# Kernel tuning notes

Hardware: AMD Instinct MI355X
Metric: run time of the kernel (lower is better)

The kernel has to match this reference:

```python
import jax, jax.numpy as jnp
import numpy as np

N_C, N_F = 25000, 100000   # coarse / fine node counts
E_C, E_F = 100000, 400000  # coarse / fine edge counts
W, F_IN, F_OUT = 128, 128, 4


def _fnn2(x, w1, b1, w2, b2):
    # 2-layer FNN (fnns_depth=2) with SELU, dropout=0 (eval)
    return jax.nn.selu(x @ w1 + b1) @ w2 + b2


def _interaction(v, e, src, dst, n, ew1, eb1, ew2, eb2, nw1, nb1, nw2, nb2):
    # InteractionNetwork: edge update (gather) -> mean scatter -> node update, residuals
    e = _fnn2(jnp.concatenate([e, v[src], v[dst]], axis=-1), ew1, eb1, ew2, eb2) + e
    s = jax.ops.segment_sum(e, dst, num_segments=n)
    cnt = jax.ops.segment_sum(jnp.ones((e.shape[0], 1), e.dtype), dst, num_segments=n)
    agg = s / jnp.maximum(cnt, 1.0)  # 'mean' aggregation
    v = _fnn2(jnp.concatenate([v, agg], axis=-1), nw1, nb1, nw2, nb2) + v
    return v, e


def setup_inputs() -> dict:
    key = jax.random.key(0)
    ks = iter(jax.random.split(key, 64))
    def rn(shape, scale=1.0):
        return jax.random.normal(next(ks), shape, jnp.float32) * scale
    s3, s2, s1 = 1.0 / np.sqrt(3 * W), 1.0 / np.sqrt(2 * W), 1.0 / np.sqrt(W)
    d = {
        'v': rn((N_C, F_IN)),
        'c_coarse': rn((N_C, W)), 'c_fine': rn((N_F, W)),
        'e_coarse': rn((E_C, W)), 'e_fine': rn((E_F, W)),
        'rel_dist': rn((N_F, 1)),
        'ei_coarse': jax.random.randint(next(ks), (2, E_C), 0, N_C),
        'ei_fine': jax.random.randint(next(ks), (2, E_F), 0, N_F),
        'cluster': jax.random.randint(next(ks), (N_F,), 0, N_C),
        'in_node_w': rn((F_IN, W), 1.0 / np.sqrt(F_IN)), 'in_node_b': rn((W,), 0.01),
        'cond_w': rn((2, W, W), s1), 'cond_b': rn((2, W), 0.01),
        'edge_in_w': rn((2, W, W), s1), 'edge_in_b': rn((2, W), 0.01),
        'bn_ew1': rn((2, 3 * W, W), s3), 'bn_eb1': rn((2, W), 0.01),
        'bn_ew2': rn((2, W, W), s1), 'bn_eb2': rn((2, W), 0.01),
        'bn_nw1': rn((2, 2 * W, W), s2), 'bn_nb1': rn((2, W), 0.01),
        'bn_nw2': rn((2, W, W), s1), 'bn_nb2': rn((2, W), 0.01),
        'unp_w1': rn((W + 1, W), 1.0 / np.sqrt(W + 1)), 'unp_b1': rn((W,), 0.01),
        'unp_w2': rn((W, W), s1), 'unp_b2': rn((W,), 0.01),
        'up_ew1': rn((2, 3 * W, W), s3), 'up_eb1': rn((2, W), 0.01),
        'up_ew2': rn((2, W, W), s1), 'up_eb2': rn((2, W), 0.01),
        'up_nw1': rn((2, 2 * W, W), s2), 'up_nb1': rn((2, W), 0.01),
        'up_nw2': rn((2, W, W), s1), 'up_nb2': rn((2, W), 0.01),
        'out_w': rn((W, F_OUT), s1), 'out_b': rn((F_OUT,), 0.01),
    }
    return d


def reference(v, c_coarse, c_fine, e_coarse, e_fine, rel_dist, ei_coarse, ei_fine, cluster,
              in_node_w, in_node_b, cond_w, cond_b, edge_in_w, edge_in_b,
              bn_ew1, bn_eb1, bn_ew2, bn_eb2, bn_nw1, bn_nb1, bn_nw2, bn_nb2,
              unp_w1, unp_b1, unp_w2, unp_b2,
              up_ew1, up_eb1, up_ew2, up_eb2, up_nw1, up_nb1, up_nw2, up_nb2,
              out_w, out_b):
    src_c, dst_c = ei_coarse[0], ei_coarse[1]
    src_f, dst_f = ei_fine[0], ei_fine[1]
    # input projection + coarse-scale conditioning
    v = v @ in_node_w + in_node_b
    v = v + (c_coarse @ cond_w[0] + cond_b[0])
    e = e_coarse @ edge_in_w[0] + edge_in_b[0]
    # bottleneck InteractionNetwork blocks on coarse graph
    for i in range(bn_ew1.shape[0]):
        v, e = _interaction(v, e, src_c, dst_c, N_C,
                            bn_ew1[i], bn_eb1[i], bn_ew2[i], bn_eb2[i],
                            bn_nw1[i], bn_nb1[i], bn_nw2[i], bn_nb2[i])
    # up block: project skip conditioning/edges, unpool coarse->fine via cluster gather + FNN on [v, scalar rel pos]
    c = c_fine @ cond_w[1] + cond_b[1]
    e = e_fine @ edge_in_w[1] + edge_in_b[1]
    v = _fnn2(jnp.concatenate([v[cluster], rel_dist], axis=-1), unp_w1, unp_b1, unp_w2, unp_b2)
    v = v + c
    for i in range(up_ew1.shape[0]):
        v, e = _interaction(v, e, src_f, dst_f, N_F,
                            up_ew1[i], up_eb1[i], up_ew2[i], up_eb2[i],
                            up_nw1[i], up_nb1[i], up_nw2[i], up_nb2[i])
    return v @ out_w + out_b
```

## Files before the change

### kernel.cpp

```cpp
#include <hip/hip_runtime.h>
#include <hip/hip_bf16.h>

typedef __bf16 bf16_t;
typedef __bf16 bf16x8 __attribute__((ext_vector_type(8)));
typedef float f32x4 __attribute__((ext_vector_type(4)));

#define SELU_SCALE 1.0507009873554805f
#define SELU_ALPHA 1.6732632423543772f

__device__ __forceinline__ float selu_f(float x) {
    return x > 0.0f ? SELU_SCALE * x : SELU_SCALE * SELU_ALPHA * (__expf(x) - 1.0f);
}

__device__ __forceinline__ int4 load8(const void* p, size_t elem_off, int isf) {
    if (!isf) return *(const int4*)((const bf16_t*)p + elem_off);
    const float* f = (const float*)p + elem_off;
    float4 a = ((const float4*)f)[0], b = ((const float4*)f)[1];
    union { int4 i; bf16_t h[8]; } u;
    u.h[0] = (bf16_t)a.x; u.h[1] = (bf16_t)a.y; u.h[2] = (bf16_t)a.z; u.h[3] = (bf16_t)a.w;
    u.h[4] = (bf16_t)b.x; u.h[5] = (bf16_t)b.y; u.h[6] = (bf16_t)b.z; u.h[7] = (bf16_t)b.w;
    return u.i;
}

__global__ void detect_dtype(const unsigned short* p, int* flag) {
    if (threadIdx.x == 0) {
        float m = 0.0f;
        for (int i = 0; i < 128; i++) {
            unsigned int u = ((unsigned int)p[i]) << 16;
            float v = __uint_as_float(u);
            v = fabsf(v);
            if (!(v <= 1e3f)) { m = 1e30f; break; }
            m = fmaxf(m, v);
        }
        *flag = (m > 1e3f) ? 1 : 0;
    }
}

struct VDesc { const void* s; bf16_t* d; int eoff; int n; };
struct VArgs { VDesc v[19]; };
__global__ void convert_vecs(VArgs a, const int* __restrict__ flag) {
    int isf = *flag;
    VDesc vd = a.v[blockIdx.y];
    int i = blockIdx.x * 256 + threadIdx.x;
    if (i < vd.n) {
        size_t idx = (size_t)vd.eoff + i;
        vd.d[i] = isf ? (bf16_t)(((const float*)vd.s)[idx]) : ((const bf16_t*)vd.s)[idx];
    }
}

struct TDesc { const void* s; bf16_t* d; int eoff; int Ksrc; int Ktot; int koff; };
struct TArgs { TDesc t[31]; };
__global__ void transpose_all(TArgs a, const int* __restrict__ flag) {
    int isf = *flag;
    TDesc td = a.t[blockIdx.y];
    int i = blockIdx.x * 256 + threadIdx.x;
    if (i < 128 * td.Ksrc) {
        int n = i / td.Ksrc;
        int k = i - n * td.Ksrc;
        size_t si = (size_t)td.eoff + (size_t)k * 128 + n;
        bf16_t v = isf ? (bf16_t)(((const float*)td.s)[si]) : ((const bf16_t*)td.s)[si];
        td.d[(size_t)n * td.Ktot + td.koff + k] = v;
    }
}

__global__ void count_dst2(const int* __restrict__ d0, int* __restrict__ c0, int E0,
                           const int* __restrict__ d1, int* __restrict__ c1, int E1) {
    const int* dst = blockIdx.y ? d1 : d0;
    int* cnt = blockIdx.y ? c1 : c0;
    int E = blockIdx.y ? E1 : E0;
    int e = blockIdx.x * 256 + threadIdx.x;
    if (e < E) atomicAdd(&cnt[dst[e]], 1);
}

__global__ void seg_alloc2(const int* __restrict__ c0, int* __restrict__ rp0, int* __restrict__ cu0, int n0,
                           const int* __restrict__ c1, int* __restrict__ rp1, int* __restrict__ cu1, int n1,
                           int* __restrict__ totals) {
    const int* cnt = blockIdx.y ? c1 : c0;
    int* rp = blockIdx.y ? rp1 : rp0;
    int* cu = blockIdx.y ? cu1 : cu0;
    int n = blockIdx.y ? n1 : n0;
    int* total = totals + blockIdx.y;
    int i = blockIdx.x * 256 + threadIdx.x;
    if (i < n) { int s = atomicAdd(total, cnt[i]); rp[i] = s; cu[i] = s; }
}

__global__ void csr_scatter2(const int* __restrict__ d0, int* __restrict__ cu0, int* __restrict__ e0, int E0,
                             const int* __restrict__ d1, int* __restrict__ cu1, int* __restrict__ e1, int E1) {
    const int* dst = blockIdx.y ? d1 : d0;
    int* cur = blockIdx.y ? cu1 : cu0;
    int* eids = blockIdx.y ? e1 : e0;
    int E = blockIdx.y ? E1 : E0;
    int e = blockIdx.x * 256 + threadIdx.x;
    if (e < E) {
        unsigned s = (unsigned)atomicAdd(&cur[dst[e]], 1);
        if (s < (unsigned)E) eids[s] = e;
    }
}

__global__ void permute_ends2(const int* __restrict__ e0, const int* __restrict__ s0,
                              const int* __restrict__ d0, int* __restrict__ sp0,
                              int* __restrict__ dp0, int E0,
                              const int* __restrict__ e1, const int* __restrict__ s1,
                              const int* __restrict__ d1, int* __restrict__ sp1,
                              int* __restrict__ dp1, int E1) {
    const int* eids = blockIdx.y ? e1 : e0;
    const int* src = blockIdx.y ? s1 : s0;
    const int* dst = blockIdx.y ? d1 : d0;
    int* sp = blockIdx.y ? sp1 : sp0;
    int* dp = blockIdx.y ? dp1 : dp0;
    int E = blockIdx.y ? E1 : E0;
    int s = blockIdx.x * 256 + threadIdx.x;
    if (s < E) { int e = eids[s]; sp[s] = src[e]; dp[s] = dst[e]; }
}

template<int K, int N>
__global__ __launch_bounds__(256) void lin1(
    int M, const void* __restrict__ A0, const void* __restrict__ A1,
    const int* __restrict__ gi,
    const bf16_t* __restrict__ Wt, const bf16_t* __restrict__ b1,
    const bf16_t* __restrict__ b2, const bf16_t* __restrict__ res,
    bf16_t* __restrict__ out, const int* __restrict__ flag)
{
    constexpr int SA = K + 8;
    constexpr int NCT = N / 64;
    __shared__ bf16_t sA[64 * SA];
    const int isf = *flag;
    const int tid = threadIdx.x;
    const int row0 = blockIdx.x * 64;
    const int lane16 = tid & 15;
    const int rgrp = tid >> 4;

    #pragma unroll
    for (int chunk = 0; chunk < K; chunk += 128) {
        const void* sp = chunk ? A1 : A0;
        for (int r = rgrp; r < 64; r += 16) {
            int rr = row0 + r; if (rr >= M) rr = M - 1;
            if (gi) rr = gi[rr];
            int4 u = load8(sp, (size_t)rr * 128 + lane16 * 8, isf);
            *(int4*)&sA[r * SA + chunk + lane16 * 8] = u;
        }
    }
    __syncthreads();

    const int lane = tid & 63, wave = tid >> 6;
    const int l15 = lane & 15, lk = lane >> 4;
    const int colbase = wave * (N / 4);
    f32x4 acc[4][NCT];
    const f32x4 zero = {0.f, 0.f, 0.f, 0.f};
    for (int rt = 0; rt < 4; rt++)
        for (int ct = 0; ct < NCT; ct++) acc[rt][ct] = zero;

    #pragma unroll
    for (int k0 = 0; k0 < K; k0 += 32) {
        bf16x8 wv[NCT];
        #pragma unroll
        for (int ct = 0; ct < NCT; ct++)
            wv[ct] = *(const bf16x8*)(Wt + (size_t)(colbase + ct * 16 + l15) * K + k0 + lk * 8);
        #pragma unroll
        for (int rt = 0; rt < 4; rt++) {
            bf16x8 av = *(const bf16x8*)(&sA[(rt * 16 + l15) * SA + k0 + lk * 8]);
            #pragma unroll
            for (int ct = 0; ct < NCT; ct++)
                acc[rt][ct] = __builtin_amdgcn_mfma_f32_16x16x32_bf16(av, wv[ct], acc[rt][ct], 0, 0, 0);
        }
    }

    #pragma unroll
    for (int rt = 0; rt < 4; rt++)
        #pragma unroll
        for (int ct = 0; ct < NCT; ct++) {
            int col = colbase + ct * 16 + l15;
            float bc = (float)b1[col] + (b2 ? (float)b2[col] : 0.0f);
            #pragma unroll
            for (int r = 0; r < 4; r++) {
                int grow = row0 + rt * 16 + lk * 4 + r;
                if (grow < M) {
                    float x = acc[rt][ct][r] + bc;
                    if (res) x += (float)res[(size_t)grow * N + col];
                    out[(size_t)grow * N + col] = (bf16_t)x;
                }
            }
        }
}

template<int MODE>
__global__ __launch_bounds__(512, 8) void fnn2k(
    int M,
    const bf16_t* __restrict__ A0, const bf16_t* __restrict__ Psd,
    const int* __restrict__ g0, const int* __restrict__ g1,
    const bf16_t* __restrict__ Emat, const int* __restrict__ rp,
    const int* __restrict__ degc,
    const bf16_t* __restrict__ W1t, const bf16_t* __restrict__ b1,
    const bf16_t* __restrict__ W2t, const bf16_t* __restrict__ b2,
    const bf16_t* __restrict__ relb, const bf16_t* __restrict__ w1last,
    const bf16_t* __restrict__ res, bf16_t* __restrict__ out,
    const bf16_t* __restrict__ finw, const bf16_t* __restrict__ finb,
    void* __restrict__ fout, const int* __restrict__ flag)
{
    constexpr int NP = (MODE == 3) ? 1 : 2;
    constexpr int K1 = (MODE == 2) ? 256 : 128;
    constexpr int PL = 64 * 136;
    __shared__ bf16_t sA[NP * PL];
    bf16_t* sH = sA + (NP - 1) * PL;

    const int isf = *flag;
    const int tid = threadIdx.x;
    const int lane16 = tid & 15;
    const int rgrp = tid >> 4;
    const int lane = tid & 63, wave = tid >> 6;
    const int l15 = lane & 15, lk = lane >> 4;
    const int colbase = wave * 16;
    const int row0 = blockIdx.x * 64;
    const bool res_lds = (res == A0);
    const f32x4 zero = {0.f, 0.f, 0.f, 0.f};

    #pragma unroll
    for (int c = 0; c < NP; c++) {
        #pragma unroll
        for (int i = 0; i < 2; i++) {
            int r = rgrp + i * 32;
            int rr = row0 + r; if (rr >= M) rr = M - 1;
            int4 u;
            if (MODE == 1 && c == 1) {
                bf16x8 pa = *(const bf16x8*)(Psd + (size_t)g0[rr] * 256 + lane16 * 8);
                bf16x8 pb = *(const bf16x8*)(Psd + (size_t)g1[rr] * 256 + 128 + lane16 * 8);
                union { int4 i4; bf16_t h[8]; } w;
                #pragma unroll
                for (int j = 0; j < 8; j++) w.h[j] = (bf16_t)((float)pa[j] + (float)pb[j]);
                u = w.i4;
            } else if (MODE == 2 && c == 1) {
                int beg = rp[rr], deg = degc[rr];
                float a8[8] = {0.f, 0.f, 0.f, 0.f, 0.f, 0.f, 0.f, 0.f};
                const bf16_t* ep = Emat + (size_t)beg * 128 + lane16 * 8;
                for (int e = 0; e < deg; e++) {
                    bf16x8 ev = *(const bf16x8*)ep;
                    ep += 128;
                    #pragma unroll
                    for (int j = 0; j < 8; j++) a8[j] += (float)ev[j];
                }
                float inv = 1.0f / (float)(deg > 0 ? deg : 1);
                union { int4 i4; bf16_t h[8]; } w;
                #pragma unroll
                for (int j = 0; j < 8; j++) w.h[j] = (bf16_t)(a8[j] * inv);
                u = w.i4;
            } else {
                const bf16_t* sp = (MODE == 3) ? A0 + (size_t)g0[rr] * 128
                                               : A0 + (size_t)rr * 128;
                u = *(const int4*)(sp + lane16 * 8);
            }
            *(int4*)&sA[c * PL + r * 136 + lane16 * 8] = u;
        }
    }
    __syncthreads();

    f32x4 acc[4];
    #pragma unroll
    for (int rt = 0; rt < 4; rt++) acc[rt] = zero;
    #pragma unroll
    for (int k0 = 0; k0 < K1; k0 += 32) {
        bf16x8 w0 = *(const bf16x8*)(W1t + (size_t)(colbase + l15) * K1 + k0 + lk * 8);
        #pragma unroll
        for (int rt = 0; rt < 4; rt++) {
            bf16x8 av = *(const bf16x8*)(&sA[(k0 / 128) * PL + (rt * 16 + l15) * 136 + (k0 & 127) + lk * 8]);
            acc[rt] = __builtin_amdgcn_mfma_f32_16x16x32_bf16(av, w0, acc[rt], 0, 0, 0);
        }
    }
    if (MODE != 1) __syncthreads();

    {
        int col = colbase + l15;
        float b1c = (float)b1[col];
        float wlc = (MODE == 3) ? (float)w1last[col] : 0.0f;
        #pragma unroll
        for (int rt = 0; rt < 4; rt++)
            #pragma unroll
            for (int r = 0; r < 4; r++) {
                int lrow = rt * 16 + lk * 4 + r;
                int grow = row0 + lrow;
                float x = acc[rt][r] + b1c;
                if (MODE == 1) x += (float)sH[lrow * 136 + col];
                if (MODE == 3) {
                    float rv = (grow < M) ? (float)relb[grow] : 0.0f;
                    x += rv * wlc;
                }
                x = selu_f(x);
                sH[lrow * 136 + col] = (bf16_t)x;
            }
    }
    __syncthreads();

    f32x4 acc2[4];
    #pragma unroll
    for (int rt = 0; rt < 4; rt++) acc2[rt] = zero;
    #pragma unroll
    for (int k0 = 0; k0 < 128; k0 += 32) {
        bf16x8 w0 = *(const bf16x8*)(W2t + (size_t)(colbase + l15) * 128 + k0 + lk * 8);
        #pragma unroll
        for (int rt = 0; rt < 4; rt++) {
            bf16x8 av = *(const bf16x8*)(&sH[(rt * 16 + l15) * 136 + k0 + lk * 8]);
            acc2[rt] = __builtin_amdgcn_mfma_f32_16x16x32_bf16(av, w0, acc2[rt], 0, 0, 0);
        }
    }
    if (finw) __syncthreads();

    {
        int col = colbase + l15;
        float b2c = (float)b2[col];
        #pragma unroll
        for (int rt = 0; rt < 4; rt++)
            #pragma unroll
            for (int r = 0; r < 4; r++) {
                int lrow = rt * 16 + lk * 4 + r;
                int grow = row0 + lrow;
                if (grow < M) {
                    float x = acc2[rt][r] + b2c;
                    if (res) {
                        float rv = (res_lds && NP > 1) ? (float)sA[lrow * 136 + col]
                                                       : (float)res[(size_t)grow * 128 + col];
                        x += rv;
                    }
                    bf16_t xb = (bf16_t)x;
                    if (out) out[(size_t)grow * 128 + col] = xb;
                    if (finw) sH[lrow * 136 + col] = xb;
                }
            }
    }

    if (finw) {
        __syncthreads();
        if (tid < 256) {
            int orow = tid >> 2, c = tid & 3;
            int grow = row0 + orow;
            if (grow < M) {
                float s = (float)finb[c];
                #pragma unroll
                for (int k = 0; k < 128; k++)
                    s += (float)sH[orow * 136 + k] * (float)finw[k * 4 + c];
                if (isf) ((float*)fout)[(size_t)grow * 4 + c] = s;
                else     ((bf16_t*)fout)[(size_t)grow * 4 + c] = (bf16_t)s;
            }
        }
    }
}

extern "C" void kernel_launch(void* const* d_in, const int* in_sizes, int n_in,
                              void* d_out, int out_size, void* d_ws, size_t ws_size,
                              hipStream_t stream) {
    const int NC = 25000, NF = 100000, EC = 100000, EF = 400000;

    const void* v_in      = d_in[0];
    const void* c_coarse  = d_in[1];
    const void* c_fine    = d_in[2];
    const void* e_coarse  = d_in[3];
    const void* e_fine    = d_in[4];
    const void* rel_dist  = d_in[5];
    const int*  ei_c      = (const int*)d_in[6];
    const int*  ei_f      = (const int*)d_in[7];
    const int*  cluster   = (const int*)d_in[8];
    const void* in_node_w = d_in[9];
    const void* in_node_b = d_in[10];
    const void* cond_w    = d_in[11];
    const void* cond_b    = d_in[12];
    const void* edge_in_w = d_in[13];
    const void* edge_in_b = d_in[14];
    const void* bn_ew1    = d_in[15];
    const void* bn_eb1    = d_in[16];
    const void* bn_ew2    = d_in[17];
    const void* bn_eb2    = d_in[18];
    const void* bn_nw1    = d_in[19];
    const void* bn_nb1    = d_in[20];
    const void* bn_nw2    = d_in[21];
    const void* bn_nb2    = d_in[22];
    const void* unp_w1    = d_in[23];
    const void* unp_b1    = d_in[24];
    const void* unp_w2    = d_in[25];
    const void* unp_b2    = d_in[26];
    const void* up_ew1    = d_in[27];
    const void* up_eb1    = d_in[28];
    const void* up_ew2    = d_in[29];
    const void* up_eb2    = d_in[30];
    const void* up_nw1    = d_in[31];
    const void* up_nb1    = d_in[32];
    const void* up_nw2    = d_in[33];
    const void* up_nb2    = d_in[34];
    const void* out_w     = d_in[35];
    const void* out_b     = d_in[36];

    const int* src_c = ei_c, * dst_c = ei_c + EC;
    const int* src_f = ei_f, * dst_f = ei_f + EF;

    char* base = (char*)d_ws;
    size_t off = 0;
    auto carve = [&](size_t bytes) -> void* {
        void* p = base + off;
        off += (bytes + 255) & ~(size_t)255;
        return p;
    };
    int*    flag   = (int*)carve(256);
    int*    zflag  = (int*)carve(256);
    int*    totals = (int*)carve(256);
    bf16_t* vc     = (bf16_t*)carve((size_t)NC * 128 * 2);
    bf16_t* vf     = (bf16_t*)carve((size_t)NF * 128 * 2);
    bf16_t* ef     = (bf16_t*)carve((size_t)EF * 128 * 2);
    bf16_t* ec     = ef;
    bf16_t* Psd    = (bf16_t*)carve((size_t)NF * 256 * 2);
    int*    cnti_c = (int*)carve((size_t)NC * 4);
    int*    cnti_f = (int*)carve((size_t)NF * 4);
    int*    rp_c   = (int*)carve((size_t)NC * 4);
    int*    rp_f   = (int*)carve((size_t)NF * 4);
    int*    cur_c  = (int*)carve((size_t)NC * 4);
    int*    cur_f  = (int*)carve((size_t)NF * 4);
    int*    srcp_c = (int*)carve((size_t)EC * 4);
    int*    dstp_c = (int*)carve((size_t)EC * 4);
    int*    srcp_f = (int*)carve((size_t)EF * 4);
    int*    dstp_f = (int*)carve((size_t)EF * 4);

    auto cw = [&](size_t elems) -> bf16_t* { return (bf16_t*)carve(elems * 2); };
    bf16_t* Wic    = cw(128 * 256);
    bf16_t* Wein0  = cw(128 * 128);
    bf16_t* Wein1  = cw(128 * 128);
    bf16_t* Wcond1 = cw(128 * 128);
    bf16_t* Wbe1[2] = { cw(128 * 128), cw(128 * 128) };
    bf16_t* Wsd_c[2] = { cw(256 * 128), cw(256 * 128) };
    bf16_t* Wbe2[2] = { cw(128 * 128), cw(128 * 128) };
    bf16_t* Wbn1[2] = { cw(128 * 256), cw(128 * 256) };
    bf16_t* Wbn2[2] = { cw(128 * 128), cw(128 * 128) };
    bf16_t* Wunp1 = cw(128 * 128);
    bf16_t* Wunp2 = cw(128 * 128);
    bf16_t* Wue1[2] = { cw(128 * 128), cw(128 * 128) };
    bf16_t* Wsd_f[2] = { cw(256 * 128), cw(256 * 128) };
    bf16_t* Wue2[2] = { cw(128 * 128), cw(128 * 128) };
    bf16_t* Wun1[2] = { cw(128 * 256), cw(128 * 256) };
    bf16_t* Wun2[2] = { cw(128 * 128), cw(128 * 128) };
    bf16_t* b_in   = cw(128);
    bf16_t* b_cond = cw(256);
    bf16_t* b_ein  = cw(256);
    bf16_t* b_be1  = cw(256);
    bf16_t* b_be2  = cw(256);
    bf16_t* b_bn1  = cw(256);
    bf16_t* b_bn2  = cw(256);
    bf16_t* b_unp1 = cw(128);
    bf16_t* b_unp2 = cw(128);
    bf16_t* b_ue1  = cw(256);
    bf16_t* b_ue2  = cw(256);
    bf16_t* b_un1  = cw(256);
    bf16_t* b_un2  = cw(256);
    bf16_t* b_out  = cw(8);
    bf16_t* w1last = cw(128);
    bf16_t* relb   = cw(NF);
    bf16_t* foutw  = cw(512);
    bf16_t* zerob  = cw(256);
    int*    eids_c = (int*)carve((size_t)EC * 4);
    int*    eids_f = (int*)carve((size_t)EF * 4);

    detect_dtype<<<1, 64, 0, stream>>>((const unsigned short*)in_node_b, flag);
    hipMemsetAsync(zflag, 0, 256, stream);
    hipMemsetAsync(zerob, 0, 512, stream);

    VArgs va; int vi = 0;
    auto addV = [&](const void* s, bf16_t* d, int eoff, int n) {
        va.v[vi].s = s; va.v[vi].d = d; va.v[vi].eoff = eoff; va.v[vi].n = n; vi++;
    };
    addV(in_node_b, b_in, 0, 128);
    addV(cond_b, b_cond, 0, 256);
    addV(edge_in_b, b_ein, 0, 256);
    addV(bn_eb1, b_be1, 0, 256);  addV(bn_eb2, b_be2, 0, 256);
    addV(bn_nb1, b_bn1, 0, 256);  addV(bn_nb2, b_bn2, 0, 256);
    addV(unp_b1, b_unp1, 0, 128); addV(unp_b2, b_unp2, 0, 128);
    addV(up_eb1, b_ue1, 0, 256);  addV(up_eb2, b_ue2, 0, 256);
    addV(up_nb1, b_un1, 0, 256);  addV(up_nb2, b_un2, 0, 256);
    addV(out_b, b_out, 0, 4);
    addV(unp_w1, w1last, 128 * 128, 128);
    addV(rel_dist, relb, 0, NF);
    addV(out_w, foutw, 0, 512);
    dim3 vg((NF + 255) / 256, vi);
    convert_vecs<<<vg, 256, 0, stream>>>(va, flag);

    TArgs ta; int ti = 0;
    auto addT = [&](const void* s, bf16_t* d, int eoff, int Ksrc, int Ktot, int koff) {
        ta.t[ti].s = s; ta.t[ti].d = d; ta.t[ti].eoff = eoff;
        ta.t[ti].Ksrc = Ksrc; ta.t[ti].Ktot = Ktot; ta.t[ti].koff = koff; ti++;
    };
    addT(in_node_w, Wic, 0, 128, 256, 0);
    addT(cond_w,    Wic, 0, 128, 256, 128);
    addT(edge_in_w, Wein0, 0, 128, 128, 0);
    addT(edge_in_w, Wein1, 16384, 128, 128, 0);
    addT(cond_w,    Wcond1, 16384, 128, 128, 0);
    for (int i = 0; i < 2; i++) {
        addT(bn_ew1, Wbe1[i],           i * 49152,         128, 128, 0);
        addT(bn_ew1, Wsd_c[i],          i * 49152 + 16384, 128, 128, 0);
        addT(bn_ew1, Wsd_c[i] + 16384,  i * 49152 + 32768, 128, 128, 0);
        addT(bn_ew2, Wbe2[i], i * 16384, 128, 128, 0);
        addT(bn_nw1, Wbn1[i], i * 32768, 256, 256, 0);
        addT(bn_nw2, Wbn2[i], i * 16384, 128, 128, 0);
        addT(up_ew1, Wue1[i],           i * 49152,         128, 128, 0);
        addT(up_ew1, Wsd_f[i],          i * 49152 + 16384, 128, 128, 0);
        addT(up_ew1, Wsd_f[i] + 16384,  i * 49152 + 32768, 128, 128, 0);
        addT(up_ew2, Wue2[i], i * 16384, 128, 128, 0);
        addT(up_nw1, Wun1[i], i * 32768, 256, 256, 0);
        addT(up_nw2, Wun2[i], i * 16384, 128, 128, 0);
    }
    addT(unp_w1, Wunp1, 0, 128, 128, 0);
    addT(unp_w2, Wunp2, 0, 128, 128, 0);
    dim3 tg((128 * 256 + 255) / 256, ti);
    transpose_all<<<tg, 256, 0, stream>>>(ta, flag);

    hipMemsetAsync(cnti_c, 0, (size_t)NC * 4, stream);
    hipMemsetAsync(cnti_f, 0, (size_t)NF * 4, stream);
    hipMemsetAsync(totals, 0, 256, stream);
    dim3 ge((EF + 255) / 256, 2), gn((NF + 255) / 256, 2);
    count_dst2<<<ge, 256, 0, stream>>>(dst_c, cnti_c, EC, dst_f, cnti_f, EF);
    seg_alloc2<<<gn, 256, 0, stream>>>(cnti_c, rp_c, cur_c, NC, cnti_f, rp_f, cur_f, NF, totals);
    csr_scatter2<<<ge, 256, 0, stream>>>(dst_c, cur_c, eids_c, EC, dst_f, cur_f, eids_f, EF);
    permute_ends2<<<ge, 256, 0, stream>>>(eids_c, src_c, dst_c, srcp_c, dstp_c, EC,
                                          eids_f, src_f, dst_f, srcp_f, dstp_f, EF);

    lin1<256, 128><<<(NC + 63) / 64, 256, 0, stream>>>(NC, v_in, c_coarse, nullptr, Wic,
                                                       b_in, b_cond, nullptr, vc, flag);
    lin1<128, 128><<<(EC + 63) / 64, 256, 0, stream>>>(EC, e_coarse, nullptr, eids_c, Wein0,
                                                       b_ein, nullptr, nullptr, ec, flag);

    for (int i = 0; i < 2; i++) {
        lin1<128, 256><<<(NC + 63) / 64, 256, 0, stream>>>(NC, vc, nullptr, nullptr, Wsd_c[i],
                                                           zerob, nullptr, nullptr, Psd, zflag);
        fnn2k<1><<<(EC + 63) / 64, 512, 0, stream>>>(
            EC, ec, Psd, srcp_c, dstp_c, nullptr, nullptr, nullptr,
            Wbe1[i], b_be1 + i * 128, Wbe2[i], b_be2 + i * 128,
            nullptr, nullptr, ec, ec, nullptr, nullptr, nullptr, flag);
        fnn2k<2><<<(NC + 63) / 64, 512, 0, stream>>>(
            NC, vc, nullptr, nullptr, nullptr, ec, rp_c, cnti_c,
            Wbn1[i], b_bn1 + i * 128, Wbn2[i], b_bn2 + i * 128,
            nullptr, nullptr, vc, vc, nullptr, nullptr, nullptr, flag);
    }

    lin1<128, 128><<<(NF + 63) / 64, 256, 0, stream>>>(NF, c_fine, nullptr, nullptr, Wcond1,
                                                       b_cond + 128, nullptr, nullptr, vf, flag);
    fnn2k<3><<<(NF + 63) / 64, 512, 0, stream>>>(
        NF, vc, nullptr, cluster, nullptr, nullptr, nullptr, nullptr,
        Wunp1, b_unp1, Wunp2, b_unp2,
        relb, w1last, vf, vf, nullptr, nullptr, nullptr, flag);
    lin1<128, 128><<<(EF + 63) / 64, 256, 0, stream>>>(EF, e_fine, nullptr, eids_f, Wein1,
                                                       b_ein + 128, nullptr, nullptr, ef, flag);

    for (int i = 0; i < 2; i++) {
        lin1<128, 256><<<(NF + 63) / 64, 256, 0, stream>>>(NF, vf, nullptr, nullptr, Wsd_f[i],
                                                           zerob, nullptr, nullptr, Psd, zflag);
        fnn2k<1><<<(EF + 63) / 64, 512, 0, stream>>>(
            EF, ef, Psd, srcp_f, dstp_f, nullptr, nullptr, nullptr,
            Wue1[i], b_ue1 + i * 128, Wue2[i], b_ue2 + i * 128,
            nullptr, nullptr, ef, ef, nullptr, nullptr, nullptr, flag);
        int last = (i == 1);
        fnn2k<2><<<(NF + 63) / 64, 512, 0, stream>>>(
            NF, vf, nullptr, nullptr, nullptr, ef, rp_f, cnti_f,
            Wun1[i], b_un1 + i * 128, Wun2[i], b_un2 + i * 128,
            nullptr, nullptr, vf, (last ? nullptr : vf),
            (last ? foutw : nullptr), b_out,
            (last ? d_out : nullptr), flag);
    }
}
```

Baseline: 782.6 us.

## Fuse edge and conditioning input projections into first interaction and unpool kernels

Adds an INPROJ template path to fnn2k that loads raw edge features (permuted via eids) or fine conditioning features and applies the input linear projection in-kernel with MFMA. This lets the first edge update consume the projected edges directly, and lets the unpool kernel add the conditioning term from registers. The separate lin1 launches for the edge input projections and the c_fine conditioning are removed. That cuts kernel launches and the write/read round-trip of the projected ec/ef/vf tensors, at the cost of extra per-block MFMA work, an extra LDS plane in MODE 3, and more register pressure.

Measured after the change: 729.2 us (median of 2 runs). 1.07x faster.

```diff
diff --git a/kernel.cpp b/kernel.cpp
--- a/kernel.cpp
+++ b/kernel.cpp
@@ -183,13 +183,15 @@
         }
 }
 
-template<int MODE>
+template<int MODE, int INPROJ>
 __global__ __launch_bounds__(512, 8) void fnn2k(
     int M,
     const bf16_t* __restrict__ A0, const bf16_t* __restrict__ Psd,
     const int* __restrict__ g0, const int* __restrict__ g1,
     const bf16_t* __restrict__ Emat, const int* __restrict__ rp,
     const int* __restrict__ degc,
+    const void* __restrict__ Araw, const int* __restrict__ gie,
+    const bf16_t* __restrict__ W0t, const bf16_t* __restrict__ b0,
     const bf16_t* __restrict__ W1t, const bf16_t* __restrict__ b1,
     const bf16_t* __restrict__ W2t, const bf16_t* __restrict__ b2,
     const bf16_t* __restrict__ relb, const bf16_t* __restrict__ w1last,
@@ -197,7 +199,7 @@
     const bf16_t* __restrict__ finw, const bf16_t* __restrict__ finb,
     void* __restrict__ fout, const int* __restrict__ flag)
 {
-    constexpr int NP = (MODE == 3) ? 1 : 2;
+    constexpr int NP = (MODE == 3 && !INPROJ) ? 1 : 2;
     constexpr int K1 = (MODE == 2) ? 256 : 128;
     constexpr int PL = 64 * 136;
     __shared__ bf16_t sA[NP * PL];
@@ -221,7 +223,10 @@
             int r = rgrp + i * 32;
             int rr = row0 + r; if (rr >= M) rr = M - 1;
             int4 u;
-            if (MODE == 1 && c == 1) {
+            if (MODE == 1 && INPROJ && c == 0) {
+                int rr2 = gie[rr];
+                u = load8(Araw, (size_t)rr2 * 128 + lane16 * 8, isf);
+            } else if (MODE == 1 && c == 1) {
                 bf16x8 pa = *(const bf16x8*)(Psd + (size_t)g0[rr] * 256 + lane16 * 8);
                 bf16x8 pb = *(const bf16x8*)(Psd + (size_t)g1[rr] * 256 + 128 + lane16 * 8);
                 union { int4 i4; bf16_t h[8]; } w;
@@ -243,6 +248,8 @@
                 #pragma unroll
                 for (int j = 0; j < 8; j++) w.h[j] = (bf16_t)(a8[j] * inv);
                 u = w.i4;
+            } else if (MODE == 3 && c == 1) {
+                u = load8(Araw, (size_t)rr * 128 + lane16 * 8, isf);
             } else {
                 const bf16_t* sp = (MODE == 3) ? A0 + (size_t)g0[rr] * 128
                                                : A0 + (size_t)rr * 128;
@@ -252,6 +259,41 @@
         }
     }
     __syncthreads();
+
+    f32x4 cC[4] = {zero, zero, zero, zero};
+    if constexpr (INPROJ) {
+        constexpr int PX = (MODE == 1) ? 0 : 1;
+        f32x4 a0r[4];
+        #pragma unroll
+        for (int rt = 0; rt < 4; rt++) a0r[rt] = zero;
+        #pragma unroll
+        for (int k0 = 0; k0 < 128; k0 += 32) {
+            bf16x8 w0 = *(const bf16x8*)(W0t + (size_t)(colbase + l15) * 128 + k0 + lk * 8);
+            #pragma unroll
+            for (int rt = 0; rt < 4; rt++) {
+                bf16x8 av = *(const bf16x8*)(&sA[PX * PL + (rt * 16 + l15) * 136 + k0 + lk * 8]);
+                a0r[rt] = __builtin_amdgcn_mfma_f32_16x16x32_bf16(av, w0, a0r[rt], 0, 0, 0);
+            }
+        }
+        __syncthreads();
+        int col = colbase + l15;
+        float b0c = (float)b0[col];
+        if constexpr (MODE == 1) {
+            #pragma unroll
+            for (int rt = 0; rt < 4; rt++)
+                #pragma unroll
+                for (int r = 0; r < 4; r++) {
+                    int lrow = rt * 16 + lk * 4 + r;
+                    sA[lrow * 136 + col] = (bf16_t)(a0r[rt][r] + b0c);
+                }
+            __syncthreads();
+        } else {
+            #pragma unroll
+            for (int rt = 0; rt < 4; rt++)
+                #pragma unroll
+                for (int r = 0; r < 4; r++) cC[rt][r] = a0r[rt][r] + b0c;
+        }
+    }
 
     f32x4 acc[4];
     #pragma unroll
@@ -314,10 +356,17 @@
                 int grow = row0 + lrow;
                 if (grow < M) {
                     float x = acc2[rt][r] + b2c;
-                    if (res) {
-                        float rv = (res_lds && NP > 1) ? (float)sA[lrow * 136 + col]
-                                                       : (float)res[(size_t)grow * 128 + col];
-                        x += rv;
+                    if constexpr (MODE == 3 && INPROJ) {
+                        x += cC[rt][r];
+                    }
+                    if constexpr (MODE == 1 && INPROJ) {
+                        x += (float)sA[lrow * 136 + col];
+                    } else {
+                        if (res) {
+                            float rv = (res_lds && NP > 1) ? (float)sA[lrow * 136 + col]
+                                                           : (float)res[(size_t)grow * 128 + col];
+                            x += rv;
+                        }
                     }
                     bf16_t xb = (bf16_t)x;
                     if (out) out[(size_t)grow * 128 + col] = xb;
@@ -517,44 +566,61 @@
 
     lin1<256, 128><<<(NC + 63) / 64, 256, 0, stream>>>(NC, v_in, c_coarse, nullptr, Wic,
                                                        b_in, b_cond, nullptr, vc, flag);
-    lin1<128, 128><<<(EC + 63) / 64, 256, 0, stream>>>(EC, e_coarse, nullptr, eids_c, Wein0,
-                                                       b_ein, nullptr, nullptr, ec, flag);
-
-    for (int i = 0; i < 2; i++) {
-        lin1<128, 256><<<(NC + 63) / 64, 256, 0, stream>>>(NC, vc, nullptr, nullptr, Wsd_c[i],
-                                                           zerob, nullptr, nullptr, Psd, zflag);
-        fnn2k<1><<<(EC + 63) / 64, 512, 0, stream>>>(
-            EC, ec, Psd, srcp_c, dstp_c, nullptr, nullptr, nullptr,
-            Wbe1[i], b_be1 + i * 128, Wbe2[i], b_be2 + i * 128,
-            nullptr, nullptr, ec, ec, nullptr, nullptr, nullptr, flag);
-        fnn2k<2><<<(NC + 63) / 64, 512, 0, stream>>>(
-            NC, vc, nullptr, nullptr, nullptr, ec, rp_c, cnti_c,
-            Wbn1[i], b_bn1 + i * 128, Wbn2[i], b_bn2 + i * 128,
-            nullptr, nullptr, vc, vc, nullptr, nullptr, nullptr, flag);
-    }
-
-    lin1<128, 128><<<(NF + 63) / 64, 256, 0, stream>>>(NF, c_fine, nullptr, nullptr, Wcond1,
-                                                       b_cond + 128, nullptr, nullptr, vf, flag);
-    fnn2k<3><<<(NF + 63) / 64, 512, 0, stream>>>(
+
+    lin1<128, 256><<<(NC + 63) / 64, 256, 0, stream>>>(NC, vc, nullptr, nullptr, Wsd_c[0],
+                                                       zerob, nullptr, nullptr, Psd, zflag);
+    fnn2k<1, 1><<<(EC + 63) / 64, 512, 0, stream>>>(
+        EC, nullptr, Psd, srcp_c, dstp_c, nullptr, nullptr, nullptr,
+        e_coarse, eids_c, Wein0, b_ein,
+        Wbe1[0], b_be1, Wbe2[0], b_be2,
+        nullptr, nullptr, nullptr, ec, nullptr, nullptr, nullptr, flag);
+    fnn2k<2, 0><<<(NC + 63) / 64, 512, 0, stream>>>(
+        NC, vc, nullptr, nullptr, nullptr, ec, rp_c, cnti_c,
+        nullptr, nullptr, nullptr, nullptr,
+        Wbn1[0], b_bn1, Wbn2[0], b_bn2,
+        nullptr, nullptr, vc, vc, nullptr, nullptr, nullptr, flag);
+    lin1<128, 256><<<(NC + 63) / 64, 256, 0, stream>>>(NC, vc, nullptr, nullptr, Wsd_c[1],
+                                                       zerob, nullptr, nullptr, Psd, zflag);
+    fnn2k<1, 0><<<(EC + 63) / 64, 512, 0, stream>>>(
+        EC, ec, Psd, srcp_c, dstp_c, nullptr, nullptr, nullptr,
+        nullptr, nullptr, nullptr, nullptr,
+        Wbe1[1], b_be1 + 128, Wbe2[1], b_be2 + 128,
+        nullptr, nullptr, ec, ec, nullptr, nullptr, nullptr, flag);
+    fnn2k<2, 0><<<(NC + 63) / 64, 512, 0, stream>>>(
+        NC, vc, nullptr, nullptr, nullptr, ec, rp_c, cnti_c,
+        nullptr, nullptr, nullptr, nullptr,
+        Wbn1[1], b_bn1 + 128, Wbn2[1], b_bn2 + 128,
+        nullptr, nullptr, vc, vc, nullptr, nullptr, nullptr, flag);
+
+    fnn2k<3, 1><<<(NF + 63) / 64, 512, 0, stream>>>(
         NF, vc, nullptr, cluster, nullptr, nullptr, nullptr, nullptr,
+        c_fine, nullptr, Wcond1, b_cond + 128,
         Wunp1, b_unp1, Wunp2, b_unp2,
-        relb, w1last, vf, vf, nullptr, nullptr, nullptr, flag);
-    lin1<128, 128><<<(EF + 63) / 64, 256, 0, stream>>>(EF, e_fine, nullptr, eids_f, Wein1,
-                                                       b_ein + 128, nullptr, nullptr, ef, flag);
-
-    for (int i = 0; i < 2; i++) {
-        lin1<128, 256><<<(NF + 63) / 64, 256, 0, stream>>>(NF, vf, nullptr, nullptr, Wsd_f[i],
-                                                           zerob, nullptr, nullptr, Psd, zflag);
-        fnn2k<1><<<(EF + 63) / 64, 512, 0, stream>>>(
-            EF, ef, Psd, srcp_f, dstp_f, nullptr, nullptr, nullptr,
-            Wue1[i], b_ue1 + i * 128, Wue2[i], b_ue2 + i * 128,
-            nullptr, nullptr, ef, ef, nullptr, nullptr, nullptr, flag);
-        int last = (i == 1);
-        fnn2k<2><<<(NF + 63) / 64, 512, 0, stream>>>(
-            NF, vf, nullptr, nullptr, nullptr, ef, rp_f, cnti_f,
-            Wun1[i], b_un1 + i * 128, Wun2[i], b_un2 + i * 128,
-            nullptr, nullptr, vf, (last ? nullptr : vf),
-            (last ? foutw : nullptr), b_out,
-            (last ? d_out : nullptr), flag);
-    }
-}
+        relb, w1last, nullptr, vf, nullptr, nullptr, nullptr, flag);
+
+    lin1<128, 256><<<(NF + 63) / 64, 256, 0, stream>>>(NF, vf, nullptr, nullptr, Wsd_f[0],
+                                                       zerob, nullptr, nullptr, Psd, zflag);
+    fnn2k<1, 1><<<(EF + 63) / 64, 512, 0, stream>>>(
+        EF, nullptr, Psd, srcp_f, dstp_f, nullptr, nullptr, nullptr,
+        e_fine, eids_f, Wein1, b_ein + 128,
+        Wue1[0], b_ue1, Wue2[0], b_ue2,
+        nullptr, nullptr, nullptr, ef, nullptr, nullptr, nullptr, flag);
+    fnn2k<2, 0><<<(NF + 63) / 64, 512, 0, stream>>>(
+        NF, vf, nullptr, nullptr, nullptr, ef, rp_f, cnti_f,
+        nullptr, nullptr, nullptr, nullptr,
+        Wun1[0], b_un1, Wun2[0], b_un2,
+        nullptr, nullptr, vf, vf, nullptr, nullptr, nullptr, flag);
+    lin1<128, 256><<<(NF + 63) / 64, 256, 0, stream>>>(NF, vf, nullptr, nullptr, Wsd_f[1],
+                                                       zerob, nullptr, nullptr, Psd, zflag);
+    fnn2k<1, 0><<<(EF + 63) / 64, 512, 0, stream>>>(
+        EF, ef, Psd, srcp_f, dstp_f, nullptr, nullptr, nullptr,
+        nullptr, nullptr, nullptr, nullptr,
+        Wue1[1], b_ue1 + 128, Wue2[1], b_ue2 + 128,
+        nullptr, nullptr, ef, ef, nullptr, nullptr, nullptr, flag);
+    fnn2k<2, 0><<<(NF + 63) / 64, 512, 0, stream>>>(
+        NF, vf, nullptr, nullptr, nullptr, ef, rp_f, cnti_f,
+        nullptr, nullptr, nullptr, nullptr,
+        Wun1[1], b_un1 + 128, Wun2[1], b_un2 + 128,
+        nullptr, nullptr, vf, nullptr,
+        foutw, b_out, d_out, flag);
+}
```
